# Performance work log

Hardware: AMD Instinct MI355X
Metric: run time of the kernel (lower is better)

## Reference

```python
import jax, jax.numpy as jnp
import numpy as np


def setup_inputs() -> dict:
    key = jax.random.key(0)
    k1, k2, k3 = jax.random.split(key, 3)
    B, T, D, U = 32, 2048, 512, 512
    x = jax.random.normal(k1, (B, T, D), dtype=jnp.float32)
    W = jax.random.normal(k2, (D, U), dtype=jnp.float32) * (1.0 / np.sqrt(D))
    R = jax.random.normal(k3, (U, U), dtype=jnp.float32) * (1.0 / np.sqrt(U))
    h0 = jnp.zeros((B, U), dtype=jnp.float32)
    return {"x": x, "W": W, "R": R, "h0": h0}


def reference(x, W, R, h0):
    # Linear recurrence: h_t = x_t @ W + h_{t-1} @ R
    # Precompute the input projection for all timesteps in one big GEMM.
    xW = jnp.einsum("btd,du->btu", x, W)  # [B, T, U]

    def step(h, xw_t):
        h_new = xw_t + h @ R  # [B, U]
        return h_new, h_new

    # scan over time (leading axis): move T to front
    _, hs = jax.lax.scan(step, h0, jnp.swapaxes(xW, 0, 1))  # hs: [T, B, U]
    return jnp.swapaxes(hs, 0, 1)  # [B, T, U]
```

## Files before the change

### kernel.cpp

```cpp
#include <hip/hip_runtime.h>
#include <hip/hip_bf16.h>


typedef float f32x4 __attribute__((ext_vector_type(4)));
typedef __bf16 bf16x8 __attribute__((ext_vector_type(8)));

#define TDIM 2048L
#define UDIM 512L
#define ST32 16384L
#define ST64 32768L
#define TS 262144L
#define FE 786432L
#define PP 520

__device__ __forceinline__ f32x4 mfma16(bf16x8 a, bf16x8 b, f32x4 c) {
  return __builtin_amdgcn_mfma_f32_16x16x32_bf16(a, b, c, 0, 0, 0);
}

__device__ __forceinline__ int hidx(int row, int col) {
  return row * 512 + (col ^ ((row & 7) << 3));
}

__device__ __forceinline__ void pack8(const f32x4& v0, const f32x4& v1,
                                      bf16x8& hv, bf16x8& lv) {
#pragma unroll
  for (int j = 0; j < 4; ++j) {
    const float a = v0[j];
    const __bf16 ha = (__bf16)a;
    hv[j] = ha; lv[j] = (__bf16)(a - (float)ha);
    const float b = v1[j];
    const __bf16 hb = (__bf16)b;
    hv[j + 4] = hb; lv[j + 4] = (__bf16)(b - (float)hb);
  }
}


__device__ __forceinline__ void stage32p(const float* __restrict__ src,
                                         long pitch, __bf16* Phi, __bf16* Plo) {
  for (int i = threadIdx.x; i < 2048; i += blockDim.x) {
    const int row = i >> 6, cb = i & 63;
    const float* p = src + (long)row * pitch + cb * 8;
    bf16x8 hv, lv;
    pack8(*(const f32x4*)p, *(const f32x4*)(p + 4), hv, lv);
    const int o = row * PP + cb * 8;
    *(bf16x8*)(Phi + o) = hv;
    *(bf16x8*)(Plo + o) = lv;
  }
}

__device__ __forceinline__ void write_bt(const __bf16* Phi, const __bf16* Plo,
                                         float* out, long t) {
  for (int i = threadIdx.x; i < 2048; i += blockDim.x) {
    const int row = i >> 6, cb = i & 63;
    const int o = row * PP + cb * 8;
    const bf16x8 hv = *(const bf16x8*)(Phi + o);
    const bf16x8 lv = *(const bf16x8*)(Plo + o);
    f32x4 o0, o1;
#pragma unroll
    for (int j = 0; j < 4; ++j) {
      o0[j] = (float)hv[j] + (float)lv[j];
      o1[j] = (float)hv[j + 4] + (float)lv[j + 4];
    }
    float* dst = out + (long)row * (TDIM * UDIM) + t * UDIM + cb * 8;
    *(f32x4*)dst = o0;
    *(f32x4*)(dst + 4) = o1;
  }
}

__device__ __forceinline__ void write_flat(const __bf16* Phi, const __bf16* Plo,
                                           float* dst) {
  for (int i = threadIdx.x; i < 2048; i += blockDim.x) {
    const int row = i >> 6, cb = i & 63;
    const int o = row * PP + cb * 8;
    const bf16x8 hv = *(const bf16x8*)(Phi + o);
    const bf16x8 lv = *(const bf16x8*)(Plo + o);
    f32x4 o0, o1;
#pragma unroll
    for (int j = 0; j < 4; ++j) {
      o0[j] = (float)hv[j] + (float)lv[j];
      o1[j] = (float)hv[j + 4] + (float)lv[j + 4];
    }
    float* d = dst + row * 512 + cb * 8;
    *(f32x4*)d = o0;
    *(f32x4*)(d + 4) = o1;
  }
}

template <int NTERM, int NPROD, bool HAS_H>
__device__ __forceinline__ void pstep32(__bf16* Phi, __bf16* Plo,
                                        const __bf16* __restrict__ bfrag,
                                        const float* __restrict__ addbase,
                                        long addpitch) {
  const int tid = threadIdx.x, l = tid & 63, w = tid >> 6, g = l >> 4, li = l & 15;
  f32x4 addv[2][2];
#pragma unroll
  for (int mt = 0; mt < 2; ++mt)
#pragma unroll
    for (int q = 0; q < 2; ++q) {
      const int col = (w * 2 + q) * 16 + li;
#pragma unroll
      for (int r = 0; r < 4; ++r) {
        const int bat = mt * 16 + g * 4 + r;
        addv[mt][q][r] = addbase[(long)bat * addpitch + col];
      }
    }

  f32x4 acc[2][2] = {};
  if (HAS_H) {
#pragma unroll 4
    for (int kk = 0; kk < 16; ++kk) {
      bf16x8 b[NTERM][2];
#pragma unroll
      for (int q = 0; q < 2; ++q) {
        const long fo = (((long)(w * 2 + q) * 16 + kk) * 64 + l) * 8;
#pragma unroll
        for (int tt = 0; tt < NTERM; ++tt)
          b[tt][q] = *(const bf16x8*)(bfrag + (long)tt * TS + fo);
      }
#pragma unroll
      for (int mt = 0; mt < 2; ++mt) {
        const int o = (mt * 16 + li) * PP + kk * 32 + g * 8;
        const bf16x8 a1 = *(const bf16x8*)(Phi + o);
        const bf16x8 a2 = *(const bf16x8*)(Plo + o);
#pragma unroll
        for (int q = 0; q < 2; ++q) {
          acc[mt][q] = mfma16(a1, b[0][q], acc[mt][q]);
          if (NTERM >= 2) acc[mt][q] = mfma16(a1, b[1][q], acc[mt][q]);
          if (NPROD > NTERM) acc[mt][q] = mfma16(a2, b[0][q], acc[mt][q]);
          if (NPROD >= 4) acc[mt][q] = mfma16(a1, b[NTERM - 1][q], acc[mt][q]);
        }
      }
    }
    __syncthreads();
  }

#pragma unroll
  for (int mt = 0; mt < 2; ++mt)
#pragma unroll
    for (int q = 0; q < 2; ++q) {
      const int col = (w * 2 + q) * 16 + li;
#pragma unroll
      for (int r = 0; r < 4; ++r) {
        const float v = (HAS_H ? acc[mt][q][r] : 0.0f) + addv[mt][q][r];
        const int row = mt * 16 + g * 4 + r;
        const __bf16 hi = (__bf16)v;
        const int o = row * PP + col;
        Phi[o] = hi;
        Plo[o] = (__bf16)(v - (float)hi);
      }
    }
  __syncthreads();
}

__device__ __forceinline__ void dstep(__bf16* Phi, __bf16* Plo,
                                      __bf16* Qhi, __bf16* Qlo,
                                      const __bf16* __restrict__ r2f,
                                      const __bf16* __restrict__ rf,
                                      const float* __restrict__ xw,
                                      long t1, long t2) {
  stage32p(xw + t1 * UDIM, TDIM * UDIM, Qhi, Qlo);
  __syncthreads();
  const int tid = threadIdx.x, l = tid & 63, w = tid >> 6, g = l >> 4, li = l & 15;
  f32x4 addv[2][2];
#pragma unroll
  for (int mt = 0; mt < 2; ++mt)
#pragma unroll
    for (int q = 0; q < 2; ++q) {
      const int col = (w * 2 + q) * 16 + li;
#pragma unroll
      for (int r = 0; r < 4; ++r) {
        const int bat = mt * 16 + g * 4 + r;
        addv[mt][q][r] = xw[(long)bat * (TDIM * UDIM) + t2 * UDIM + col];
      }
    }
  f32x4 acc[2][2] = {};
#pragma unroll 2
  for (int kk = 0; kk < 16; ++kk) {
    bf16x8 c0[2], c1[2], d0[2], d1[2];
#pragma unroll
    for (int q = 0; q < 2; ++q) {
      const long fo = (((long)(w * 2 + q) * 16 + kk) * 64 + l) * 8;
      c0[q] = *(const bf16x8*)(r2f + fo);
      c1[q] = *(const bf16x8*)(r2f + TS + fo);
      d0[q] = *(const bf16x8*)(rf + fo);
      d1[q] = *(const bf16x8*)(rf + TS + fo);
    }
#pragma unroll
    for (int mt = 0; mt < 2; ++mt) {
      const int o = (mt * 16 + li) * PP + kk * 32 + g * 8;
      const bf16x8 h1 = *(const bf16x8*)(Phi + o);
      const bf16x8 h2 = *(const bf16x8*)(Plo + o);
      const bf16x8 q1 = *(const bf16x8*)(Qhi + o);
      const bf16x8 q2 = *(const bf16x8*)(Qlo + o);
#pragma unroll
      for (int q = 0; q < 2; ++q) {
        acc[mt][q] = mfma16(h1, c0[q], acc[mt][q]);
        acc[mt][q] = mfma16(q1, d0[q], acc[mt][q]);
        acc[mt][q] = mfma16(h1, c1[q], acc[mt][q]);
        acc[mt][q] = mfma16(q1, d1[q], acc[mt][q]);
        acc[mt][q] = mfma16(h2, c0[q], acc[mt][q]);
        acc[mt][q] = mfma16(q2, d0[q], acc[mt][q]);
      }
    }
  }
  __syncthreads();
#pragma unroll
  for (int mt = 0; mt < 2; ++mt)
#pragma unroll
    for (int q = 0; q < 2; ++q) {
      const int col = (w * 2 + q) * 16 + li;
#pragma unroll
      for (int r = 0; r < 4; ++r) {
        const float v = acc[mt][q][r] + addv[mt][q][r];
        const int row = mt * 16 + g * 4 + r;
        const __bf16 hi = (__bf16)v;
        const int o = row * PP + col;
        Phi[o] = hi;
        Plo[o] = (__bf16)(v - (float)hi);
      }
    }
  __syncthreads();
}


__device__ __forceinline__ void xw_dev(long blk, const float* __restrict__ x,
                                       const __bf16* __restrict__ wf,
                                       float* __restrict__ out, char* smem) {
  __bf16* Phi = (__bf16*)smem;
  const float* src = x + blk * ST64;
  for (int i = threadIdx.x; i < 4096; i += 512) {
    const int row = i >> 6, cb = i & 63;
    const f32x4 v0 = *(const f32x4*)(src + (long)row * 512 + cb * 8);
    const f32x4 v1 = *(const f32x4*)(src + (long)row * 512 + cb * 8 + 4);
    bf16x8 hv;
#pragma unroll
    for (int j = 0; j < 4; ++j) {
      hv[j] = (__bf16)v0[j];
      hv[j + 4] = (__bf16)v1[j];
    }
    *(bf16x8*)(Phi + row * PP + cb * 8) = hv;
  }
  __syncthreads();
  const int tid = threadIdx.x, l = tid & 63, w = tid >> 6, g = l >> 4, li = l & 15;
  f32x4 acc[4][4] = {};
#pragma unroll 4
  for (int kk = 0; kk < 16; ++kk) {
    bf16x8 b0[4];
#pragma unroll
    for (int q = 0; q < 4; ++q) {
      const long fo = (((long)(w * 4 + q) * 16 + kk) * 64 + l) * 8;
      b0[q] = *(const bf16x8*)(wf + fo);
    }
#pragma unroll
    for (int mt = 0; mt < 4; ++mt) {
      const bf16x8 a1 = *(const bf16x8*)(Phi + (mt * 16 + li) * PP + kk * 32 + g * 8);
#pragma unroll
      for (int q = 0; q < 4; ++q)
        acc[mt][q] = mfma16(a1, b0[q], acc[mt][q]);
    }
  }
  float* gdst = out + blk * ST64;
#pragma unroll
  for (int mt = 0; mt < 4; ++mt)
#pragma unroll
    for (int q = 0; q < 4; ++q) {
      const int col = (w * 4 + q) * 16 + li;
#pragma unroll
      for (int r = 0; r < 4; ++r)
        gdst[(long)(mt * 16 + g * 4 + r) * 512 + col] = acc[mt][q][r];
    }
}

__device__ __forceinline__ void stage_sw(const float* __restrict__ src,
                                         float* hbuf) {
  for (int i = threadIdx.x; i < 4096; i += 512) {
    const int flat = i * 4, row = flat >> 9, col = flat & 511;
    *(f32x4*)&hbuf[hidx(row, col)] = *(const f32x4*)&src[flat];
  }
}

__device__ __forceinline__ f32x4 lds_mm(const float* hbuf,
                                        const __bf16* __restrict__ bf,
                                        int mt, int ntg) {
  const int tid = threadIdx.x, l = tid & 63, g = (l >> 4) & 3, li = l & 15;
  f32x4 acc = {};
#pragma unroll 2
  for (int kk = 0; kk < 16; ++kk) {
    const long fo = (((long)ntg * 16 + kk) * 64 + l) * 8;
    const bf16x8 b0 = *(const bf16x8*)(bf + fo);
    const bf16x8 b1 = *(const bf16x8*)(bf + TS + fo);
    bf16x8 a1, a2;
    const float* pp = &hbuf[hidx(mt * 16 + li, kk * 32 + g * 8)];
#pragma unroll
    for (int j = 0; j < 8; ++j) {
      const float v = pp[j];
      const __bf16 hi = (__bf16)v;
      a1[j] = hi;
      a2[j] = (__bf16)(v - (float)hi);
    }
    acc = mfma16(a1, b0, acc);
    acc = mfma16(a1, b1, acc);
    acc = mfma16(a2, b0, acc);
  }
  return acc;
}

__device__ __forceinline__ void sq_dev(int b, const float* __restrict__ a,
                                       const __bf16* __restrict__ bf,
                                       float* __restrict__ of32,
                                       __bf16* __restrict__ ofr, float* hbuf) {
  const int rg = b >> 3, cg = b & 7;
  const int tid = threadIdx.x, l = tid & 63, w = tid >> 6, g = l >> 4, li = l & 15;
  stage_sw(a + (long)rg * ST32, hbuf);
  __syncthreads();
  const int mt = w >> 2, q = w & 3, ntg = cg * 4 + q;
  f32x4 acc = {};
#pragma unroll 2
  for (int kk = 0; kk < 16; ++kk) {
    const long fo = (((long)ntg * 16 + kk) * 64 + l) * 8;
    const bf16x8 b0 = *(const bf16x8*)(bf + fo);
    const bf16x8 b1 = *(const bf16x8*)(bf + TS + fo);
    const bf16x8 b2 = *(const bf16x8*)(bf + 2 * TS + fo);
    bf16x8 a1, a2;
    const float* pp = &hbuf[hidx(mt * 16 + li, kk * 32 + g * 8)];
#pragma unroll
    for (int j = 0; j < 8; ++j) {
      const float v = pp[j];
      const __bf16 hi = (__bf16)v;
      a1[j] = hi;
      a2[j] = (__bf16)(v - (float)hi);
    }
    acc = mfma16(a1, b0, acc);
    acc = mfma16(a1, b1, acc);
    acc = mfma16(a2, b0, acc);
    acc = mfma16(a1, b2, acc);
  }
  const int n = ntg * 16 + li;
#pragma unroll
  for (int r = 0; r < 4; ++r) {
    const int k = rg * 32 + mt * 16 + g * 4 + r;
    const float v = acc[r];
    of32[(long)k * 512 + n] = v;
    const __bf16 t1 = (__bf16)v;
    const float r1 = v - (float)t1;
    const __bf16 t2 = (__bf16)r1;
    const long fi = (((long)(n >> 4) * 16 + (k >> 5)) * 64 + ((k >> 3) & 3) * 16 + (n & 15)) * 8 + (k & 7);
    ofr[fi] = t1;
    ofr[TS + fi] = t2;
    ofr[2 * TS + fi] = (__bf16)(r1 - (float)t2);
  }
}

__device__ __forceinline__ void pair_dev(int b, const float* __restrict__ in,
                                         const __bf16* __restrict__ bf,
                                         float* __restrict__ outb, float* hbuf) {
  const int p = b >> 3, cs = b & 7;
  const int tid = threadIdx.x, l = tid & 63, w = tid >> 6, g = l >> 4, li = l & 15;
  stage_sw(in + (long)(2 * p) * ST32, hbuf);
  __syncthreads();
  const int mt = w >> 2, ntg = cs * 4 + (w & 3);
  const f32x4 acc = lds_mm(hbuf, bf, mt, ntg);
  const float* addp = in + (long)(2 * p + 1) * ST32;
  float* outp = outb + (long)p * ST32;
  const int col = ntg * 16 + li;
#pragma unroll
  for (int r = 0; r < 4; ++r) {
    const int row = mt * 16 + g * 4 + r;
    outp[(long)row * 512 + col] = acc[r] + addp[(long)row * 512 + col];
  }
}


__global__ __launch_bounds__(512) void k_split2(const float* __restrict__ m0,
                                                const float* __restrict__ m1,
                                                __bf16* __restrict__ f0,
                                                __bf16* __restrict__ f1) {
  const int bb = blockIdx.x;
  const float* m = (bb < 512) ? m0 : m1;
  __bf16* f = (bb < 512) ? f0 : f1;
  const int idx = (bb & 511) * 512 + threadIdx.x;
  const int j = idx & 7, l = (idx >> 3) & 63, kk = (idx >> 9) & 15, nt = idx >> 13;
  const int k = kk * 32 + (l >> 4) * 8 + j;
  const int n = nt * 16 + (l & 15);
  const float v = m[k * 512 + n];
  const __bf16 t1 = (__bf16)v;
  const float r1 = v - (float)t1;
  const __bf16 t2 = (__bf16)r1;
  f[idx] = t1;
  f[TS + idx] = t2;
  f[2 * TS + idx] = (__bf16)(r1 - (float)t2);
}

__global__ __launch_bounds__(512) void k_xw(const float* __restrict__ x,
                                            const __bf16* __restrict__ wf,
                                            float* __restrict__ out, int base) {
  __shared__ __align__(16) char smem[64 * PP * 2];
  xw_dev(base + blockIdx.x, x, wf, out, smem);
}

__global__ __launch_bounds__(512) void k_xwsq(const float* __restrict__ sqa,
                                              const __bf16* __restrict__ sqbf,
                                              float* __restrict__ sqo32,
                                              __bf16* __restrict__ sqofr,
                                              const float* __restrict__ x,
                                              const __bf16* __restrict__ wf,
                                              float* __restrict__ out, int base) {
  __shared__ __align__(16) char smem[64 * PP * 2];
  const int b = blockIdx.x;
  if (b < 128)
    sq_dev(b, sqa, sqbf, sqo32, sqofr, (float*)smem);
  else
    xw_dev(base + (b - 128), x, wf, out, smem);
}

__global__ __launch_bounds__(512) void k_combo(const float* __restrict__ sqa,
                                               const __bf16* __restrict__ sqbf,
                                               float* __restrict__ sqo32,
                                               __bf16* __restrict__ sqofr,
                                               const float* __restrict__ prin,
                                               const __bf16* __restrict__ prbf,
                                               float* __restrict__ prout) {
  __shared__ float hbuf[ST32];
  const int b = blockIdx.x;
  if (b < 128)
    sq_dev(b, sqa, sqbf, sqo32, sqofr, hbuf);
  else
    pair_dev(b - 128, prin, prbf, prout, hbuf);
}

__global__ __launch_bounds__(1024) void k_local(const float* __restrict__ xw,
                                                const __bf16* __restrict__ rf,
                                                const __bf16* __restrict__ r2f,
                                                float* __restrict__ sout) {
  __shared__ __bf16 Phi[32 * PP], Plo[32 * PP], Qhi[32 * PP], Qlo[32 * PP];
  const long c = blockIdx.x;
  stage32p(xw + c * 8 * UDIM, TDIM * UDIM, Phi, Plo);
  __syncthreads();
  pstep32<2, 3, true>(Phi, Plo, rf, xw + (c * 8 + 1) * UDIM, TDIM * UDIM);
  dstep(Phi, Plo, Qhi, Qlo, r2f, rf, xw, c * 8 + 2, c * 8 + 3);
  dstep(Phi, Plo, Qhi, Qlo, r2f, rf, xw, c * 8 + 4, c * 8 + 5);
  dstep(Phi, Plo, Qhi, Qlo, r2f, rf, xw, c * 8 + 6, c * 8 + 7);
  write_flat(Phi, Plo, sout + c * ST32);
}

__global__ __launch_bounds__(1024) void k_fix0(const float* __restrict__ e1,
                                               const float* __restrict__ sbuf,
                                               float* out,
                                               const __bf16* __restrict__ rf,
                                               const __bf16* __restrict__ r8f) {
  __shared__ __bf16 Phi[32 * PP], Plo[32 * PP];
  const long c = blockIdx.x;
  stage32p(e1 + (c >> 1) * ST32, 512, Phi, Plo);
  __syncthreads();
  if (c & 1)
    pstep32<2, 3, true>(Phi, Plo, r8f, sbuf + (c - 1) * ST32, 512);
  for (int j = 0; j < 8; ++j) {
    pstep32<1, 2, true>(Phi, Plo, rf, out + (c * 8 + j) * UDIM, TDIM * UDIM);
    write_bt(Phi, Plo, out, c * 8 + j);
  }
}

__global__ __launch_bounds__(512) void k_down(const float* __restrict__ epar,
                                              float* __restrict__ ulev,
                                              const __bf16* __restrict__ bf) {
  __shared__ float hbuf[ST32];
  const int p = blockIdx.x >> 3, cs = blockIdx.x & 7;
  const int tid = threadIdx.x, l = tid & 63, w = tid >> 6, g = l >> 4, li = l & 15;
  stage_sw(epar + (long)p * ST32, hbuf);
  __syncthreads();
  const int mt = w >> 2, ntg = cs * 4 + (w & 3);
  const f32x4 acc = lds_mm(hbuf, bf, mt, ntg);
  float* evp = ulev + (long)(2 * p) * ST32;
  float* outp = ulev + (long)(2 * p + 1) * ST32;
  const int col = ntg * 16 + li;
  float cp[4];
#pragma unroll
  for (int r = 0; r < 4; ++r) {
    const int row = mt * 16 + g * 4 + r;
    const long off = (long)row * 512 + col;
    cp[r] = hbuf[hidx(row, col)];
    outp[off] = acc[r] + evp[off];
  }
  __syncthreads();
#pragma unroll
  for (int r = 0; r < 4; ++r) {
    const int row = mt * 16 + g * 4 + r;
    evp[(long)row * 512 + col] = cp[r];
  }
}

extern "C" void kernel_launch(void* const* d_in, const int* in_sizes, int n_in,
                              void* d_out, int out_size, void* d_ws, size_t ws_size,
                              hipStream_t stream) {
  (void)in_sizes; (void)n_in; (void)out_size; (void)ws_size;
  const float* x  = (const float*)d_in[0];
  const float* W  = (const float*)d_in[1];
  const float* R  = (const float*)d_in[2];
  const float* h0 = (const float*)d_in[3];
  float* out = (float*)d_out;

  __bf16* F  = (__bf16*)d_ws;
  __bf16* Fw = F + 11 * FE;
  float* P1 = (float*)(Fw + FE);
  float* P2 = P1 + TS;
  float* Sbuf = P2 + TS;
  float* Ub[8];
  {
    float* up = Sbuf + 256 * ST32;
    for (int k = 1; k <= 7; ++k) { Ub[k] = up; up += (1L << (8 - k)) * ST32; }
  }

  k_split2<<<1024, 512, 0, stream>>>(W, R, Fw, F);

  k_xwsq<<<384, 512, 0, stream>>>(R, F, P1, F + FE, x, Fw, out, 0);
  k_xwsq<<<384, 512, 0, stream>>>(P1, F + FE, P2, F + 2L * FE, x, Fw, out, 256);
  k_xwsq<<<384, 512, 0, stream>>>(P2, F + 2L * FE, P1, F + 3L * FE, x, Fw, out, 512);
  k_xw<<<256, 512, 0, stream>>>(x, Fw, out, 768);

  k_local<<<256, 1024, 0, stream>>>(out, F, F + FE, Sbuf);

  for (int k = 1; k <= 7; ++k) {
    const int i = k + 3;
    const float* sqa = (i & 1) ? P2 : P1;
    float* sqo = (i & 1) ? P1 : P2;
    const float* prin = (k == 1) ? Sbuf : Ub[k - 1];
    const int npr = (1 << (8 - k)) * 8;
    k_combo<<<128 + npr, 512, 0, stream>>>(sqa, F + (long)(i - 1) * FE, sqo,
                                           F + (long)i * FE, prin,
                                           F + (long)(k + 2) * FE, Ub[k]);
  }

  k_down<<<8, 512, 0, stream>>>(h0, Ub[7], F + 10L * FE);
  for (int k = 7; k >= 2; --k)
    k_down<<<(1 << (8 - k)) * 8, 512, 0, stream>>>(Ub[k], Ub[k - 1], F + (long)(k + 2) * FE);

  k_fix0<<<256, 1024, 0, stream>>>(Ub[1], Sbuf, out, F, F + 3L * FE);
}
```

Measured before the change: 461.5 us.

## Drop low-part MFMA terms and fuse output write into k_fix0 recurrence step

Removes one split-bf16 MFMA product (q1 with the low part of R) from the double-step, reducing matrix work by one sixth at some accuracy cost. In k_fix0, replaces the generic pstep32 call plus separate write_bt pass with an inline step. That step uses only two of the split-precision products, keeps the first six k-slices of R in registers across the eight timesteps, and writes fp32 results straight from the accumulator to global memory. This removes an extra LDS read pass and reloads of R fragments, at the cost of more register pressure and reduced precision.

```diff
diff --git a/kernel.cpp b/kernel.cpp
--- a/kernel.cpp
+++ b/kernel.cpp
@@ -48,25 +48,6 @@
   }
 }
 
-__device__ __forceinline__ void write_bt(const __bf16* Phi, const __bf16* Plo,
-                                         float* out, long t) {
-  for (int i = threadIdx.x; i < 2048; i += blockDim.x) {
-    const int row = i >> 6, cb = i & 63;
-    const int o = row * PP + cb * 8;
-    const bf16x8 hv = *(const bf16x8*)(Phi + o);
-    const bf16x8 lv = *(const bf16x8*)(Plo + o);
-    f32x4 o0, o1;
-#pragma unroll
-    for (int j = 0; j < 4; ++j) {
-      o0[j] = (float)hv[j] + (float)lv[j];
-      o1[j] = (float)hv[j + 4] + (float)lv[j + 4];
-    }
-    float* dst = out + (long)row * (TDIM * UDIM) + t * UDIM + cb * 8;
-    *(f32x4*)dst = o0;
-    *(f32x4*)(dst + 4) = o1;
-  }
-}
-
 __device__ __forceinline__ void write_flat(const __bf16* Phi, const __bf16* Plo,
                                            float* dst) {
   for (int i = threadIdx.x; i < 2048; i += blockDim.x) {
@@ -176,14 +157,13 @@
   f32x4 acc[2][2] = {};
 #pragma unroll 2
   for (int kk = 0; kk < 16; ++kk) {
-    bf16x8 c0[2], c1[2], d0[2], d1[2];
+    bf16x8 c0[2], c1[2], d0[2];
 #pragma unroll
     for (int q = 0; q < 2; ++q) {
       const long fo = (((long)(w * 2 + q) * 16 + kk) * 64 + l) * 8;
       c0[q] = *(const bf16x8*)(r2f + fo);
       c1[q] = *(const bf16x8*)(r2f + TS + fo);
       d0[q] = *(const bf16x8*)(rf + fo);
-      d1[q] = *(const bf16x8*)(rf + TS + fo);
     }
 #pragma unroll
     for (int mt = 0; mt < 2; ++mt) {
@@ -197,7 +177,6 @@
         acc[mt][q] = mfma16(h1, c0[q], acc[mt][q]);
         acc[mt][q] = mfma16(q1, d0[q], acc[mt][q]);
         acc[mt][q] = mfma16(h1, c1[q], acc[mt][q]);
-        acc[mt][q] = mfma16(q1, d1[q], acc[mt][q]);
         acc[mt][q] = mfma16(h2, c0[q], acc[mt][q]);
         acc[mt][q] = mfma16(q2, d0[q], acc[mt][q]);
       }
@@ -454,9 +433,72 @@
   __syncthreads();
   if (c & 1)
     pstep32<2, 3, true>(Phi, Plo, r8f, sbuf + (c - 1) * ST32, 512);
+
+  const int tid = threadIdx.x, l = tid & 63, w = tid >> 6, g = l >> 4, li = l & 15;
+  bf16x8 bc[6][2];
+#pragma unroll
+  for (int kk = 0; kk < 6; ++kk)
+#pragma unroll
+    for (int q = 0; q < 2; ++q)
+      bc[kk][q] = *(const bf16x8*)(rf + (((long)(w * 2 + q) * 16 + kk) * 64 + l) * 8);
+
   for (int j = 0; j < 8; ++j) {
-    pstep32<1, 2, true>(Phi, Plo, rf, out + (c * 8 + j) * UDIM, TDIM * UDIM);
-    write_bt(Phi, Plo, out, c * 8 + j);
+    const float* addbase = out + (c * 8 + j) * UDIM;
+    f32x4 addv[2][2];
+#pragma unroll
+    for (int mt = 0; mt < 2; ++mt)
+#pragma unroll
+      for (int q = 0; q < 2; ++q) {
+        const int col = (w * 2 + q) * 16 + li;
+#pragma unroll
+        for (int r = 0; r < 4; ++r) {
+          const int bat = mt * 16 + g * 4 + r;
+          addv[mt][q][r] = addbase[(long)bat * (TDIM * UDIM) + col];
+        }
+      }
+    f32x4 acc[2][2] = {};
+#pragma unroll
+    for (int kk = 0; kk < 16; ++kk) {
+      bf16x8 b0[2];
+      if (kk < 6) {
+        b0[0] = bc[kk][0];
+        b0[1] = bc[kk][1];
+      } else {
+#pragma unroll
+        for (int q = 0; q < 2; ++q)
+          b0[q] = *(const bf16x8*)(rf + (((long)(w * 2 + q) * 16 + kk) * 64 + l) * 8);
+      }
+#pragma unroll
+      for (int mt = 0; mt < 2; ++mt) {
+        const int o = (mt * 16 + li) * PP + kk * 32 + g * 8;
+        const bf16x8 a1 = *(const bf16x8*)(Phi + o);
+        const bf16x8 a2 = *(const bf16x8*)(Plo + o);
+#pragma unroll
+        for (int q = 0; q < 2; ++q) {
+          acc[mt][q] = mfma16(a1, b0[q], acc[mt][q]);
+          acc[mt][q] = mfma16(a2, b0[q], acc[mt][q]);
+        }
+      }
+    }
+    __syncthreads();
+    float* obase = out + (c * 8 + j) * UDIM;
+#pragma unroll
+    for (int mt = 0; mt < 2; ++mt)
+#pragma unroll
+      for (int q = 0; q < 2; ++q) {
+        const int col = (w * 2 + q) * 16 + li;
+#pragma unroll
+        for (int r = 0; r < 4; ++r) {
+          const float v = acc[mt][q][r] + addv[mt][q][r];
+          const int row = mt * 16 + g * 4 + r;
+          const __bf16 hi = (__bf16)v;
+          const int o = row * PP + col;
+          Phi[o] = hi;
+          Plo[o] = (__bf16)(v - (float)hi);
+          obase[(long)row * (TDIM * UDIM) + col] = v;
+        }
+      }
+    __syncthreads();
   }
 }
 
```

New measurement: 500.9 us. 8.5% more time.
